# Performance work log

Measured on AMD Instinct MI355X. Metric: run time of the kernel, lower is better.

The kernel has to match this reference:

```python
import jax, jax.numpy as jnp
import numpy as np

IN_CH = 512
HID = 512
SCALE = 1.0 / np.sqrt(16.0)  # hard-coded 16**0.5 in source, not sqrt(hidden)


def setup_inputs() -> dict:
    key = jax.random.key(0)
    ks = jax.random.split(key, 9)
    B, T = 8, 2048
    lim = 1.0 / np.sqrt(IN_CH)
    return {
        "q": jax.random.normal(ks[0], (B, T, IN_CH), dtype=jnp.float32),
        "k": jax.random.normal(ks[1], (B, T, IN_CH), dtype=jnp.float32),
        "v": jax.random.normal(ks[2], (B, T, IN_CH), dtype=jnp.float32),
        "Wq": jax.random.uniform(ks[3], (IN_CH, HID), jnp.float32, -lim, lim),
        "bq": jax.random.uniform(ks[4], (HID,), jnp.float32, -lim, lim),
        "Wk": jax.random.uniform(ks[5], (IN_CH, HID), jnp.float32, -lim, lim),
        "bk": jax.random.uniform(ks[6], (HID,), jnp.float32, -lim, lim),
        "Wv": jax.random.uniform(ks[7], (IN_CH, HID), jnp.float32, -lim, lim),
        "bv": jax.random.uniform(ks[8], (HID,), jnp.float32, -lim, lim),
    }


def reference(q, k, v, Wq, bq, Wk, bk, Wv, bv):
    # Linear projections: [B,T,F] @ [F,H] + [H]
    query = jnp.einsum("btf,fh->bth", q, Wq) + bq
    key_p = jnp.einsum("btf,fh->bth", k, Wk) + bk
    value = jnp.einsum("btf,fh->bth", v, Wv) + bv
    # energy: [B,T,T], scaled by fixed 1/sqrt(16)
    energy = jnp.einsum("bth,bsh->bts", query, key_p) * SCALE
    attn = jax.nn.softmax(energy, axis=-1)
    # weighted sum: [B,T,H]
    return jnp.einsum("bts,bsh->bth", attn, value)
```

## Files before the change

kernel.cpp:

```cpp
#include <hip/hip_runtime.h>
#include <stdint.h>

typedef __bf16 bf16;
typedef bf16 bf16x8 __attribute__((ext_vector_type(8)));
typedef float f32x4 __attribute__((ext_vector_type(4)));

#define MFMA(a, b, c) __builtin_amdgcn_mfma_f32_16x16x32_bf16(a, b, c, 0, 0, 0)

#define SCALE_L2E 0.3606737602222409f
#define M0 16.0f

__device__ __forceinline__ void gload_lds16(const void* g, void* l) {
  __builtin_amdgcn_global_load_lds(
      (const __attribute__((address_space(1))) uint32_t*)g,
      (__attribute__((address_space(3))) uint32_t*)l, 16, 0, 0);
}

__global__ void k_wtrans(const float* __restrict__ Wq, const float* __restrict__ Wk,
                         const float* __restrict__ Wv, bf16* __restrict__ Wt) {
  int idx = blockIdx.x * 256 + threadIdx.x;
  int z = idx >> 18;
  int r = idx & 262143;
  int n = r >> 9, k = r & 511;
  const float* W = (z == 0) ? Wq : (z == 1) ? Wk : Wv;
  Wt[idx] = (bf16)W[k * 512 + n];
}

__global__ __launch_bounds__(256, 4) void k_proj(
    const float* __restrict__ q, const float* __restrict__ k, const float* __restrict__ v,
    const bf16* __restrict__ Wt, const float* __restrict__ bq, const float* __restrict__ bk,
    const float* __restrict__ bv, bf16* __restrict__ Qp, bf16* __restrict__ Kp,
    bf16* __restrict__ Vtp) {
  int z = blockIdx.z;
  const float* A = (z == 0) ? q : (z == 1) ? k : v;
  const float* bias = (z == 0) ? bq : (z == 1) ? bk : bv;
  const bf16* Bw = Wt + (size_t)z * 512 * 512;

  int m0 = blockIdx.x * 128, n0 = blockIdx.y * 128;
  __shared__ bf16 As[128 * 40];
  __shared__ bf16 Bs[128 * 32];

  int tid = threadIdx.x;
  int wave = tid >> 6, lane = tid & 63, qr = lane & 15, quad = lane >> 4;
  int wm = (wave >> 1) * 64, wn = (wave & 1) * 64;

  f32x4 acc[4][4];
  for (int mi = 0; mi < 4; mi++)
    for (int ni = 0; ni < 4; ni++) acc[mi][ni] = (f32x4){0.f, 0.f, 0.f, 0.f};

  for (int k0 = 0; k0 < 512; k0 += 32) {
    __syncthreads();
    for (int i = 0; i < 2; i++) {
      int ch = i * 256 + tid;
      int row = ch >> 2, c = ch & 3;
      gload_lds16(Bw + (size_t)(n0 + row) * 512 + k0 + c * 8, &Bs[ch * 8]);
      const float4* src = (const float4*)(A + (size_t)(m0 + row) * 512 + k0 + c * 8);
      float4 x = src[0], y = src[1];
      bf16x8 t;
      t[0] = (bf16)x.x; t[1] = (bf16)x.y; t[2] = (bf16)x.z; t[3] = (bf16)x.w;
      t[4] = (bf16)y.x; t[5] = (bf16)y.y; t[6] = (bf16)y.z; t[7] = (bf16)y.w;
      *(bf16x8*)&As[row * 40 + c * 8] = t;
    }
    __syncthreads();
    bf16x8 af[4], bfv[4];
    for (int mi = 0; mi < 4; mi++)
      af[mi] = *(bf16x8*)&As[(wm + mi * 16 + qr) * 40 + quad * 8];
    for (int ni = 0; ni < 4; ni++)
      bfv[ni] = *(bf16x8*)&Bs[(wn + ni * 16 + qr) * 32 + quad * 8];
    for (int mi = 0; mi < 4; mi++)
      for (int ni = 0; ni < 4; ni++) acc[mi][ni] = MFMA(af[mi], bfv[ni], acc[mi][ni]);
  }

  if (z == 2) {
    for (int ni = 0; ni < 4; ni++) {
      int col = n0 + wn + ni * 16 + qr;
      float bz = bias[col];
      for (int mi = 0; mi < 4; mi++) {
        int rbase = m0 + wm + mi * 16 + quad * 4;
        int bb = rbase >> 11, tt = rbase & 2047;
        bf16 tmp[4];
        for (int r = 0; r < 4; r++) tmp[r] = (bf16)(acc[mi][ni][r] + bz);
        *(uint64_t*)(Vtp + ((size_t)(bb * 512 + col)) * 2048 + tt) = *(uint64_t*)tmp;
      }
    }
  } else {
    bf16* C = (z == 0) ? Qp : Kp;
    float sc = (z == 0) ? SCALE_L2E : 1.0f;
    for (int ni = 0; ni < 4; ni++) {
      int col = n0 + wn + ni * 16 + qr;
      float bz = bias[col];
      for (int mi = 0; mi < 4; mi++) {
        int rbase = m0 + wm + mi * 16 + quad * 4;
        for (int r = 0; r < 4; r++)
          C[(size_t)(rbase + r) * 512 + col] = (bf16)((acc[mi][ni][r] + bz) * sc);
      }
    }
  }
}

__global__ __launch_bounds__(256, 3) void k_qk(const bf16* __restrict__ Qp,
                                               const bf16* __restrict__ Kp,
                                               bf16* __restrict__ P,
                                               float* __restrict__ Lpart) {
  __shared__ bf16 As[128 * 32];
  __shared__ bf16 Bs[128 * 32];
  int b = blockIdx.z;
  const bf16* A = Qp + (size_t)b * 2048 * 512;
  const bf16* B = Kp + (size_t)b * 2048 * 512;
  bf16* Pb = P + (size_t)b * 2048 * 2048;
  int m0 = blockIdx.x * 128, n0 = blockIdx.y * 128;
  int tid = threadIdx.x;
  int wave = tid >> 6, lane = tid & 63, qr = lane & 15, quad = lane >> 4;
  int wm = (wave >> 1) * 64, wn = (wave & 1) * 64;

  f32x4 acc[4][4];
  for (int mi = 0; mi < 4; mi++)
    for (int ni = 0; ni < 4; ni++) acc[mi][ni] = (f32x4){0.f, 0.f, 0.f, 0.f};

  for (int k0 = 0; k0 < 512; k0 += 32) {
    __syncthreads();
    for (int i = 0; i < 2; i++) {
      int ch = i * 256 + tid;
      int row = ch >> 2, c = ch & 3;
      gload_lds16(A + (size_t)(m0 + row) * 512 + k0 + c * 8, &As[ch * 8]);
      gload_lds16(B + (size_t)(n0 + row) * 512 + k0 + c * 8, &Bs[ch * 8]);
    }
    __syncthreads();
    bf16x8 af[4], bfv[4];
    for (int mi = 0; mi < 4; mi++)
      af[mi] = *(bf16x8*)&As[(wm + mi * 16 + qr) * 32 + quad * 8];
    for (int ni = 0; ni < 4; ni++)
      bfv[ni] = *(bf16x8*)&Bs[(wn + ni * 16 + qr) * 32 + quad * 8];
    for (int mi = 0; mi < 4; mi++)
      for (int ni = 0; ni < 4; ni++) acc[mi][ni] = MFMA(af[mi], bfv[ni], acc[mi][ni]);
  }

  int slice = blockIdx.y * 2 + (wave & 1);
  float* Lp = Lpart + (size_t)slice * 16384 + b * 2048;
  for (int mi = 0; mi < 4; mi++) {
    int rowb = m0 + wm + mi * 16 + quad * 4;
    for (int r = 0; r < 4; r++) {
      float s = 0.f;
      bf16* prow = Pb + (size_t)(rowb + r) * 2048 + n0 + wn + qr;
      for (int ni = 0; ni < 4; ni++) {
        float e = exp2f(acc[mi][ni][r] - M0);
        prow[ni * 16] = (bf16)e;
        s += e;
      }
      s += __shfl_xor(s, 1);
      s += __shfl_xor(s, 2);
      s += __shfl_xor(s, 4);
      s += __shfl_xor(s, 8);
      if (qr == 0) Lp[rowb + r] = s;
    }
  }
}

__global__ void k_lred(const float* __restrict__ Lpart, float* __restrict__ Linv) {
  int i = blockIdx.x * 256 + threadIdx.x;
  float s = 0.f;
  for (int j = 0; j < 32; j++) s += Lpart[(size_t)j * 16384 + i];
  Linv[i] = 1.0f / s;
}

__global__ __launch_bounds__(256, 4) void k_pv(const bf16* __restrict__ P,
                                               const bf16* __restrict__ Vtp,
                                               const float* __restrict__ Linv,
                                               float* __restrict__ out) {
  __shared__ bf16 As[64 * 32];
  __shared__ bf16 Bs[128 * 32];
  int b = blockIdx.z;
  const bf16* A = P + (size_t)b * 2048 * 2048;
  const bf16* B = Vtp + (size_t)b * 512 * 2048;
  int m0 = blockIdx.x * 64, n0 = blockIdx.y * 128;
  int tid = threadIdx.x;
  int wave = tid >> 6, lane = tid & 63, qr = lane & 15, quad = lane >> 4;
  int wm = (wave >> 1) * 32, wn = (wave & 1) * 64;

  f32x4 acc[2][4];
  for (int mi = 0; mi < 2; mi++)
    for (int ni = 0; ni < 4; ni++) acc[mi][ni] = (f32x4){0.f, 0.f, 0.f, 0.f};

  for (int k0 = 0; k0 < 2048; k0 += 32) {
    __syncthreads();
    {
      int row = tid >> 2, c = tid & 3;
      gload_lds16(A + (size_t)(m0 + row) * 2048 + k0 + c * 8, &As[tid * 8]);
    }
    for (int i = 0; i < 2; i++) {
      int ch = i * 256 + tid;
      int row = ch >> 2, c = ch & 3;
      gload_lds16(B + (size_t)(n0 + row) * 2048 + k0 + c * 8, &Bs[ch * 8]);
    }
    __syncthreads();
    bf16x8 af[2], bfv[4];
    for (int mi = 0; mi < 2; mi++)
      af[mi] = *(bf16x8*)&As[(wm + mi * 16 + qr) * 32 + quad * 8];
    for (int ni = 0; ni < 4; ni++)
      bfv[ni] = *(bf16x8*)&Bs[(wn + ni * 16 + qr) * 32 + quad * 8];
    for (int mi = 0; mi < 2; mi++)
      for (int ni = 0; ni < 4; ni++) acc[mi][ni] = MFMA(af[mi], bfv[ni], acc[mi][ni]);
  }

  for (int mi = 0; mi < 2; mi++) {
    int rowb = m0 + wm + mi * 16 + quad * 4;
    float linv[4];
    for (int r = 0; r < 4; r++) linv[r] = Linv[b * 2048 + rowb + r];
    for (int ni = 0; ni < 4; ni++) {
      int col = n0 + wn + ni * 16 + qr;
      float* og = out + (size_t)(b * 2048 + rowb) * 512 + col;
      for (int r = 0; r < 4; r++) og[(size_t)r * 512] = acc[mi][ni][r] * linv[r];
    }
  }
}

extern "C" void kernel_launch(void* const* d_in, const int* in_sizes, int n_in,
                              void* d_out, int out_size, void* d_ws, size_t ws_size,
                              hipStream_t stream) {
  (void)in_sizes; (void)n_in; (void)out_size; (void)ws_size;
  const float* q  = (const float*)d_in[0];
  const float* k  = (const float*)d_in[1];
  const float* v  = (const float*)d_in[2];
  const float* Wq = (const float*)d_in[3];
  const float* bq = (const float*)d_in[4];
  const float* Wk = (const float*)d_in[5];
  const float* bk = (const float*)d_in[6];
  const float* Wv = (const float*)d_in[7];
  const float* bv = (const float*)d_in[8];
  float* out = (float*)d_out;

  char* ws = (char*)d_ws;
  bf16* Wt     = (bf16*)(ws);
  bf16* Qp     = (bf16*)(ws + 1572864);
  bf16* Kp     = (bf16*)(ws + 18350080);
  bf16* Vtp    = (bf16*)(ws + 35127296);
  bf16* P      = (bf16*)(ws + 51904512);
  float* Lpart = (float*)(ws + 119013376);
  float* Linv  = (float*)(ws + 121110528);

  k_wtrans<<<3072, 256, 0, stream>>>(Wq, Wk, Wv, Wt);
  k_proj<<<dim3(128, 4, 3), 256, 0, stream>>>(q, k, v, Wt, bq, bk, bv, Qp, Kp, Vtp);
  k_qk<<<dim3(16, 16, 8), 256, 0, stream>>>(Qp, Kp, P, Lpart);
  k_lred<<<64, 256, 0, stream>>>(Lpart, Linv);
  k_pv<<<dim3(32, 4, 8), 256, 0, stream>>>(P, Vtp, Linv, out);
}
```

Measured before the change: 304.7 us.

## Widen K tiles with XOR-swizzled LDS, tile transposes, fuse row-sum reduction into PV

Every GEMM kernel now loads 64-wide K slices into XOR-swizzled shared memory, which halves the barrier count per K step and avoids LDS bank conflicts. The PV kernel grows to 128x128 output tiles and computes the inverse softmax row sums itself, so the separate reduction launch is removed. The weight transpose uses a padded shared-memory tile so global reads and writes are coalesced, and the V-transpose output is staged through LDS for wide coalesced stores. The cost is more shared memory and registers per block (launch bounds lowered to 3), which reduces occupancy, and the PV grid has fewer blocks.

```diff
diff --git a/kernel.cpp b/kernel.cpp
--- a/kernel.cpp
+++ b/kernel.cpp
@@ -18,15 +18,19 @@
 
 __global__ void k_wtrans(const float* __restrict__ Wq, const float* __restrict__ Wk,
                          const float* __restrict__ Wv, bf16* __restrict__ Wt) {
-  int idx = blockIdx.x * 256 + threadIdx.x;
-  int z = idx >> 18;
-  int r = idx & 262143;
-  int n = r >> 9, k = r & 511;
+  __shared__ float tile[32][33];
+  int x = threadIdx.x, y = threadIdx.y;
+  int k0 = blockIdx.x * 32, n0 = blockIdx.y * 32, z = blockIdx.z;
   const float* W = (z == 0) ? Wq : (z == 1) ? Wk : Wv;
-  Wt[idx] = (bf16)W[k * 512 + n];
-}
-
-__global__ __launch_bounds__(256, 4) void k_proj(
+  for (int j = 0; j < 4; j++)
+    tile[y + 8 * j][x] = W[(size_t)(k0 + y + 8 * j) * 512 + n0 + x];
+  __syncthreads();
+  bf16* o = Wt + (size_t)z * 262144;
+  for (int j = 0; j < 4; j++)
+    o[(size_t)(n0 + y + 8 * j) * 512 + k0 + x] = (bf16)tile[x][y + 8 * j];
+}
+
+__global__ __launch_bounds__(256, 3) void k_proj(
     const float* __restrict__ q, const float* __restrict__ k, const float* __restrict__ v,
     const bf16* __restrict__ Wt, const float* __restrict__ bq, const float* __restrict__ bk,
     const float* __restrict__ bv, bf16* __restrict__ Qp, bf16* __restrict__ Kp,
@@ -34,11 +38,13 @@
   int z = blockIdx.z;
   const float* A = (z == 0) ? q : (z == 1) ? k : v;
   const float* bias = (z == 0) ? bq : (z == 1) ? bk : bv;
-  const bf16* Bw = Wt + (size_t)z * 512 * 512;
+  const bf16* Bw = Wt + (size_t)z * 262144;
 
   int m0 = blockIdx.x * 128, n0 = blockIdx.y * 128;
-  __shared__ bf16 As[128 * 40];
-  __shared__ bf16 Bs[128 * 32];
+  __shared__ __align__(16) char smem[34816];
+  bf16* As = (bf16*)smem;
+  bf16* Bs = (bf16*)(smem + 18432);
+  bf16* Ts = (bf16*)smem;
 
   int tid = threadIdx.x;
   int wave = tid >> 6, lane = tid & 63, qr = lane & 15, quad = lane >> 4;
@@ -48,40 +54,54 @@
   for (int mi = 0; mi < 4; mi++)
     for (int ni = 0; ni < 4; ni++) acc[mi][ni] = (f32x4){0.f, 0.f, 0.f, 0.f};
 
-  for (int k0 = 0; k0 < 512; k0 += 32) {
-    __syncthreads();
-    for (int i = 0; i < 2; i++) {
-      int ch = i * 256 + tid;
-      int row = ch >> 2, c = ch & 3;
-      gload_lds16(Bw + (size_t)(n0 + row) * 512 + k0 + c * 8, &Bs[ch * 8]);
+  for (int k0 = 0; k0 < 512; k0 += 64) {
+    __syncthreads();
+    for (int i = 0; i < 4; i++) {
+      int ch = i * 256 + tid;
+      int row = ch >> 3, c = ch & 7;
+      int cs = c ^ (row & 7);
+      gload_lds16(Bw + (size_t)(n0 + row) * 512 + k0 + cs * 8, &Bs[ch * 8]);
       const float4* src = (const float4*)(A + (size_t)(m0 + row) * 512 + k0 + c * 8);
       float4 x = src[0], y = src[1];
       bf16x8 t;
       t[0] = (bf16)x.x; t[1] = (bf16)x.y; t[2] = (bf16)x.z; t[3] = (bf16)x.w;
       t[4] = (bf16)y.x; t[5] = (bf16)y.y; t[6] = (bf16)y.z; t[7] = (bf16)y.w;
-      *(bf16x8*)&As[row * 40 + c * 8] = t;
-    }
-    __syncthreads();
-    bf16x8 af[4], bfv[4];
-    for (int mi = 0; mi < 4; mi++)
-      af[mi] = *(bf16x8*)&As[(wm + mi * 16 + qr) * 40 + quad * 8];
-    for (int ni = 0; ni < 4; ni++)
-      bfv[ni] = *(bf16x8*)&Bs[(wn + ni * 16 + qr) * 32 + quad * 8];
-    for (int mi = 0; mi < 4; mi++)
-      for (int ni = 0; ni < 4; ni++) acc[mi][ni] = MFMA(af[mi], bfv[ni], acc[mi][ni]);
+      *(bf16x8*)&As[row * 72 + c * 8] = t;
+    }
+    __syncthreads();
+    for (int h = 0; h < 2; h++) {
+      bf16x8 af[4], bfv[4];
+      for (int mi = 0; mi < 4; mi++)
+        af[mi] = *(bf16x8*)&As[(wm + mi * 16 + qr) * 72 + h * 32 + quad * 8];
+      for (int ni = 0; ni < 4; ni++) {
+        int rr = wn + ni * 16 + qr;
+        int cc = (h * 4 + quad) ^ (rr & 7);
+        bfv[ni] = *(bf16x8*)&Bs[rr * 64 + cc * 8];
+      }
+      for (int mi = 0; mi < 4; mi++)
+        for (int ni = 0; ni < 4; ni++) acc[mi][ni] = MFMA(af[mi], bfv[ni], acc[mi][ni]);
+    }
   }
 
   if (z == 2) {
+    __syncthreads();
     for (int ni = 0; ni < 4; ni++) {
-      int col = n0 + wn + ni * 16 + qr;
-      float bz = bias[col];
-      for (int mi = 0; mi < 4; mi++) {
-        int rbase = m0 + wm + mi * 16 + quad * 4;
-        int bb = rbase >> 11, tt = rbase & 2047;
+      int hcol = wn + ni * 16 + qr;
+      float bz = bias[n0 + hcol];
+      for (int mi = 0; mi < 4; mi++) {
+        int tl = wm + mi * 16 + quad * 4;
         bf16 tmp[4];
         for (int r = 0; r < 4; r++) tmp[r] = (bf16)(acc[mi][ni][r] + bz);
-        *(uint64_t*)(Vtp + ((size_t)(bb * 512 + col)) * 2048 + tt) = *(uint64_t*)tmp;
-      }
+        *(uint64_t*)&Ts[hcol * 136 + tl] = *(uint64_t*)tmp;
+      }
+    }
+    __syncthreads();
+    int bb = m0 >> 11, t0l = m0 & 2047;
+    for (int i = 0; i < 8; i++) {
+      int ch = i * 256 + tid;
+      int row = ch >> 4, c = ch & 15;
+      *(bf16x8*)(Vtp + (size_t)(bb * 512 + n0 + row) * 2048 + t0l + c * 8) =
+          *(bf16x8*)&Ts[row * 136 + c * 8];
     }
   } else {
     bf16* C = (z == 0) ? Qp : Kp;
@@ -102,8 +122,8 @@
                                                const bf16* __restrict__ Kp,
                                                bf16* __restrict__ P,
                                                float* __restrict__ Lpart) {
-  __shared__ bf16 As[128 * 32];
-  __shared__ bf16 Bs[128 * 32];
+  __shared__ bf16 As[128 * 64];
+  __shared__ bf16 Bs[128 * 64];
   int b = blockIdx.z;
   const bf16* A = Qp + (size_t)b * 2048 * 512;
   const bf16* B = Kp + (size_t)b * 2048 * 512;
@@ -117,22 +137,31 @@
   for (int mi = 0; mi < 4; mi++)
     for (int ni = 0; ni < 4; ni++) acc[mi][ni] = (f32x4){0.f, 0.f, 0.f, 0.f};
 
-  for (int k0 = 0; k0 < 512; k0 += 32) {
-    __syncthreads();
-    for (int i = 0; i < 2; i++) {
-      int ch = i * 256 + tid;
-      int row = ch >> 2, c = ch & 3;
-      gload_lds16(A + (size_t)(m0 + row) * 512 + k0 + c * 8, &As[ch * 8]);
-      gload_lds16(B + (size_t)(n0 + row) * 512 + k0 + c * 8, &Bs[ch * 8]);
-    }
-    __syncthreads();
-    bf16x8 af[4], bfv[4];
-    for (int mi = 0; mi < 4; mi++)
-      af[mi] = *(bf16x8*)&As[(wm + mi * 16 + qr) * 32 + quad * 8];
-    for (int ni = 0; ni < 4; ni++)
-      bfv[ni] = *(bf16x8*)&Bs[(wn + ni * 16 + qr) * 32 + quad * 8];
-    for (int mi = 0; mi < 4; mi++)
-      for (int ni = 0; ni < 4; ni++) acc[mi][ni] = MFMA(af[mi], bfv[ni], acc[mi][ni]);
+  for (int k0 = 0; k0 < 512; k0 += 64) {
+    __syncthreads();
+    for (int i = 0; i < 4; i++) {
+      int ch = i * 256 + tid;
+      int row = ch >> 3, c = ch & 7;
+      int cs = c ^ (row & 7);
+      gload_lds16(A + (size_t)(m0 + row) * 512 + k0 + cs * 8, &As[ch * 8]);
+      gload_lds16(B + (size_t)(n0 + row) * 512 + k0 + cs * 8, &Bs[ch * 8]);
+    }
+    __syncthreads();
+    for (int h = 0; h < 2; h++) {
+      bf16x8 af[4], bfv[4];
+      for (int mi = 0; mi < 4; mi++) {
+        int rr = wm + mi * 16 + qr;
+        int cc = (h * 4 + quad) ^ (rr & 7);
+        af[mi] = *(bf16x8*)&As[rr * 64 + cc * 8];
+      }
+      for (int ni = 0; ni < 4; ni++) {
+        int rr = wn + ni * 16 + qr;
+        int cc = (h * 4 + quad) ^ (rr & 7);
+        bfv[ni] = *(bf16x8*)&Bs[rr * 64 + cc * 8];
+      }
+      for (int mi = 0; mi < 4; mi++)
+        for (int ni = 0; ni < 4; ni++) acc[mi][ni] = MFMA(af[mi], bfv[ni], acc[mi][ni]);
+    }
   }
 
   int slice = blockIdx.y * 2 + (wave & 1);
@@ -156,59 +185,65 @@
   }
 }
 
-__global__ void k_lred(const float* __restrict__ Lpart, float* __restrict__ Linv) {
-  int i = blockIdx.x * 256 + threadIdx.x;
-  float s = 0.f;
-  for (int j = 0; j < 32; j++) s += Lpart[(size_t)j * 16384 + i];
-  Linv[i] = 1.0f / s;
-}
-
-__global__ __launch_bounds__(256, 4) void k_pv(const bf16* __restrict__ P,
+__global__ __launch_bounds__(256, 3) void k_pv(const bf16* __restrict__ P,
                                                const bf16* __restrict__ Vtp,
-                                               const float* __restrict__ Linv,
+                                               const float* __restrict__ Lpart,
                                                float* __restrict__ out) {
-  __shared__ bf16 As[64 * 32];
-  __shared__ bf16 Bs[128 * 32];
+  __shared__ bf16 As[128 * 64];
+  __shared__ bf16 Bs[128 * 64];
+  __shared__ float Linv_s[128];
   int b = blockIdx.z;
   const bf16* A = P + (size_t)b * 2048 * 2048;
   const bf16* B = Vtp + (size_t)b * 512 * 2048;
-  int m0 = blockIdx.x * 64, n0 = blockIdx.y * 128;
+  int m0 = blockIdx.x * 128, n0 = blockIdx.y * 128;
   int tid = threadIdx.x;
   int wave = tid >> 6, lane = tid & 63, qr = lane & 15, quad = lane >> 4;
-  int wm = (wave >> 1) * 32, wn = (wave & 1) * 64;
-
-  f32x4 acc[2][4];
-  for (int mi = 0; mi < 2; mi++)
+  int wm = (wave >> 1) * 64, wn = (wave & 1) * 64;
+
+  if (tid < 128) {
+    float s = 0.f;
+    for (int j = 0; j < 32; j++) s += Lpart[(size_t)j * 16384 + b * 2048 + m0 + tid];
+    Linv_s[tid] = 1.0f / s;
+  }
+
+  f32x4 acc[4][4];
+  for (int mi = 0; mi < 4; mi++)
     for (int ni = 0; ni < 4; ni++) acc[mi][ni] = (f32x4){0.f, 0.f, 0.f, 0.f};
 
-  for (int k0 = 0; k0 < 2048; k0 += 32) {
-    __syncthreads();
-    {
-      int row = tid >> 2, c = tid & 3;
-      gload_lds16(A + (size_t)(m0 + row) * 2048 + k0 + c * 8, &As[tid * 8]);
-    }
-    for (int i = 0; i < 2; i++) {
-      int ch = i * 256 + tid;
-      int row = ch >> 2, c = ch & 3;
-      gload_lds16(B + (size_t)(n0 + row) * 2048 + k0 + c * 8, &Bs[ch * 8]);
-    }
-    __syncthreads();
-    bf16x8 af[2], bfv[4];
-    for (int mi = 0; mi < 2; mi++)
-      af[mi] = *(bf16x8*)&As[(wm + mi * 16 + qr) * 32 + quad * 8];
-    for (int ni = 0; ni < 4; ni++)
-      bfv[ni] = *(bf16x8*)&Bs[(wn + ni * 16 + qr) * 32 + quad * 8];
-    for (int mi = 0; mi < 2; mi++)
-      for (int ni = 0; ni < 4; ni++) acc[mi][ni] = MFMA(af[mi], bfv[ni], acc[mi][ni]);
-  }
-
-  for (int mi = 0; mi < 2; mi++) {
-    int rowb = m0 + wm + mi * 16 + quad * 4;
+  for (int k0 = 0; k0 < 2048; k0 += 64) {
+    __syncthreads();
+    for (int i = 0; i < 4; i++) {
+      int ch = i * 256 + tid;
+      int row = ch >> 3, c = ch & 7;
+      int cs = c ^ (row & 7);
+      gload_lds16(A + (size_t)(m0 + row) * 2048 + k0 + cs * 8, &As[ch * 8]);
+      gload_lds16(B + (size_t)(n0 + row) * 2048 + k0 + cs * 8, &Bs[ch * 8]);
+    }
+    __syncthreads();
+    for (int h = 0; h < 2; h++) {
+      bf16x8 af[4], bfv[4];
+      for (int mi = 0; mi < 4; mi++) {
+        int rr = wm + mi * 16 + qr;
+        int cc = (h * 4 + quad) ^ (rr & 7);
+        af[mi] = *(bf16x8*)&As[rr * 64 + cc * 8];
+      }
+      for (int ni = 0; ni < 4; ni++) {
+        int rr = wn + ni * 16 + qr;
+        int cc = (h * 4 + quad) ^ (rr & 7);
+        bfv[ni] = *(bf16x8*)&Bs[rr * 64 + cc * 8];
+      }
+      for (int mi = 0; mi < 4; mi++)
+        for (int ni = 0; ni < 4; ni++) acc[mi][ni] = MFMA(af[mi], bfv[ni], acc[mi][ni]);
+    }
+  }
+
+  for (int mi = 0; mi < 4; mi++) {
+    int rowl = wm + mi * 16 + quad * 4;
     float linv[4];
-    for (int r = 0; r < 4; r++) linv[r] = Linv[b * 2048 + rowb + r];
+    for (int r = 0; r < 4; r++) linv[r] = Linv_s[rowl + r];
     for (int ni = 0; ni < 4; ni++) {
       int col = n0 + wn + ni * 16 + qr;
-      float* og = out + (size_t)(b * 2048 + rowb) * 512 + col;
+      float* og = out + (size_t)(b * 2048 + m0 + rowl) * 512 + col;
       for (int r = 0; r < 4; r++) og[(size_t)r * 512] = acc[mi][ni][r] * linv[r];
     }
   }
@@ -236,11 +271,9 @@
   bf16* Vtp    = (bf16*)(ws + 35127296);
   bf16* P      = (bf16*)(ws + 51904512);
   float* Lpart = (float*)(ws + 119013376);
-  float* Linv  = (float*)(ws + 121110528);
-
-  k_wtrans<<<3072, 256, 0, stream>>>(Wq, Wk, Wv, Wt);
+
+  k_wtrans<<<dim3(16, 16, 3), dim3(32, 8, 1), 0, stream>>>(Wq, Wk, Wv, Wt);
   k_proj<<<dim3(128, 4, 3), 256, 0, stream>>>(q, k, v, Wt, bq, bk, bv, Qp, Kp, Vtp);
   k_qk<<<dim3(16, 16, 8), 256, 0, stream>>>(Qp, Kp, P, Lpart);
-  k_lred<<<64, 256, 0, stream>>>(Lpart, Linv);
-  k_pv<<<dim3(32, 4, 8), 256, 0, stream>>>(P, Vtp, Linv, out);
-}
+  k_pv<<<dim3(16, 4, 8), 256, 0, stream>>>(P, Vtp, Lpart, out);
+}
```

After: 274.8 us. 1.11x faster.
